# Optimization experiments

Hardware: AMD Instinct MI355X
Metric: run time of the kernel (lower is better)

## Reference

```python
import jax, jax.numpy as jnp
import numpy as np

B, L, T = 256, 512, 128


def setup_inputs() -> dict:
    key = jax.random.key(0)
    k1, k2, k3, k4, k5, k6 = jax.random.split(key, 6)
    inputs = jax.random.normal(k1, (B, L, T), dtype=jnp.float32)
    transitions = jax.random.normal(k2, (T, T), dtype=jnp.float32) * (2.0 / T) ** 0.5
    start_transitions = jax.random.normal(k3, (T,), dtype=jnp.float32)
    end_transitions = jax.random.normal(k4, (T,), dtype=jnp.float32)
    tags = jax.random.randint(k5, (B, L), 0, T, dtype=jnp.int32)
    lengths = jax.random.randint(k6, (B,), L // 2, L + 1, dtype=jnp.int32)
    mask = (jnp.arange(L)[None, :] < lengths[:, None]).astype(jnp.int32)
    return {"inputs": inputs, "transitions": transitions,
            "start_transitions": start_transitions, "end_transitions": end_transitions,
            "tags": tags, "mask": mask}


def _input_likelihood(logits, maskf, transitions, start_t, end_t):
    # logits [B,L,T], maskf [B,L] float
    alpha0 = start_t[None, :] + logits[:, 0]  # [B,T]

    def step(alpha, xs):
        emit, m = xs  # emit [B,T], m [B]
        inner = alpha[:, :, None] + emit[:, None, :] + transitions[None]  # [B,T,T]
        new_alpha = jax.nn.logsumexp(inner, axis=1)
        alpha = new_alpha * m[:, None] + alpha * (1.0 - m[:, None])
        return alpha, None

    xs = (jnp.swapaxes(logits[:, 1:], 0, 1), jnp.swapaxes(maskf[:, 1:], 0, 1))
    alpha, _ = jax.lax.scan(step, alpha0, xs)
    stops = alpha + end_t[None, :]
    return jax.nn.logsumexp(stops, axis=-1)  # [B]


def _joint_likelihood(logits, tags, maskf, transitions, start_t, end_t):
    b_idx = jnp.arange(logits.shape[0])
    score = start_t[tags[:, 0]]
    trans_scores = transitions[tags[:, :-1], tags[:, 1:]]  # [B,L-1]
    emit = jnp.take_along_axis(logits, tags[:, :, None], axis=2)[..., 0]  # [B,L]
    score = score + jnp.sum(trans_scores * maskf[:, 1:], axis=1)
    score = score + jnp.sum(emit[:, :-1] * maskf[:, :-1], axis=1)
    last_idx = jnp.sum(maskf, axis=1).astype(jnp.int32) - 1
    last_tags = tags[b_idx, last_idx]
    score = score + end_t[last_tags] + logits[:, -1][b_idx, last_tags] * maskf[:, -1]
    return score


def reference(inputs, transitions, start_transitions, end_transitions, tags, mask):
    maskf = mask.astype(inputs.dtype)
    log_den = _input_likelihood(inputs, maskf, transitions, start_transitions, end_transitions)
    log_num = _joint_likelihood(inputs, tags, maskf, transitions, start_transitions, end_transitions)
    return jnp.sum(log_num - log_den)
```

## Files before the change

kernel.cpp:

```cpp
#include <hip/hip_runtime.h>

#define BB 256
#define LL 512
#define TT 128
#define CH 16

typedef _Float16 h2 __attribute__((ext_vector_type(2)));

static __device__ inline h2 pkrtz(float a, float b) {
  return __builtin_bit_cast(h2, __builtin_amdgcn_cvt_pkrtz(a, b));
}

#if defined(__has_builtin)
#if __has_builtin(__builtin_amdgcn_fdot2)
#define FDOT2(a, b, c) __builtin_amdgcn_fdot2((a), (b), (c), false)
#endif
#endif
#ifndef FDOT2
static __device__ inline float fdot2_fb(h2 a, h2 b, float c) {
  return fmaf((float)a.x, (float)b.x, fmaf((float)a.y, (float)b.y, c));
}
#define FDOT2(a, b, c) fdot2_fb((a), (b), (c))
#endif

static __device__ inline float wave_max_dpp(float x) {
  int v = __float_as_int(x);
#define DPP_STEP(ctrl)                                                  \
  {                                                                     \
    int t = __builtin_amdgcn_update_dpp(v, v, (ctrl), 0xf, 0xf, false); \
    x = fmaxf(x, __int_as_float(t));                                    \
    v = __float_as_int(x);                                              \
  }
  DPP_STEP(0x111) DPP_STEP(0x112) DPP_STEP(0x114) DPP_STEP(0x118)
  DPP_STEP(0x142) DPP_STEP(0x143)
#undef DPP_STEP
  return __int_as_float(__builtin_amdgcn_readlane(v, 63));
}

static __device__ inline h2 bch2(unsigned u) { return __builtin_bit_cast(h2, u); }
static __device__ inline unsigned expbits(unsigned u) {
  return __float_as_uint(__expf(__uint_as_float(u)));
}

__global__ __launch_bounds__(256)
__attribute__((amdgpu_waves_per_eu(1, 1)))
void crf_fb_kernel(const float* __restrict__ inputs,
                   const float* __restrict__ trans,
                   const float* __restrict__ start_t,
                   const float* __restrict__ end_t,
                   const int* __restrict__ tags,
                   const int* __restrict__ mask,
                   float* __restrict__ diff) {
  const int b = blockIdx.x;
  const int tid = threadIdx.x;
  const int lane = tid & 63;
  const int wid = tid >> 6;

  __shared__ __align__(16) float fbuf[2][CH * TT];
  __shared__ __align__(16) float bbuf[2][CH * TT];
  __shared__ __align__(16) h2 g_lds[64];
  __shared__ float numA_sh, numB_sh;
  __shared__ int sb_sh;

  int lm = 0;
  const int* mk = mask + b * LL;
#pragma unroll
  for (int q = 0; q < LL / 64; ++q) lm += mk[q * 64 + lane];
#pragma unroll
  for (int d = 1; d < 64; d <<= 1) lm += __shfl_xor(lm, d);
  const int len = lm;
  const int m = (len - 1) >> 1;
  const int NC = (len - 1 - m + CH - 1) / CH;

  const float* erow = inputs + (size_t)b * LL * TT;
  const float2* er2 = (const float2*)erow;
  const float2* tr2 = (const float2*)trans;

  auto STAGE = [&](float* dst, const float* gbase) {
    const uint4* gs = (const uint4*)gbase;
    uint4* ds = (uint4*)dst;
    uint4 v[8];
#pragma unroll
    for (int q = 0; q < 8; ++q) v[q] = gs[q * 64 + lane];
#pragma unroll
    for (int q = 0; q < 8; ++q) {
      uint4 o;
      o.x = expbits(v[q].x);
      o.y = expbits(v[q].y);
      o.z = expbits(v[q].z);
      o.w = expbits(v[q].w);
      ds[q * 64 + lane] = o;
    }
  };

  int S = 0;
  float inv_sc = 1.0f;
  int cur_ex = 0;
  h2 Ea0[64], Ea1[64];
  h2 pk;

  if (wid == 0) {
#pragma unroll
    for (int p = 0; p < 64; ++p) {
      float2 r0 = tr2[(2 * p) * 64 + lane];
      float2 r1 = tr2[(2 * p + 1) * 64 + lane];
      h2 c0, c1;
      c0.x = (_Float16)__expf(r0.x);
      c0.y = (_Float16)__expf(r1.x);
      c1.x = (_Float16)__expf(r0.y);
      c1.y = (_Float16)__expf(r1.y);
      Ea0[p] = c0;
      Ea1[p] = c1;
    }
    float2 em0 = er2[lane];
    float f0 = __expf(start_t[2 * lane] + em0.x);
    float f1 = __expf(start_t[2 * lane + 1] + em0.y);
    pk = pkrtz(f0, f1);
    float mx = wave_max_dpp(fmaxf(f0, f1));
    int exm = (int)((__float_as_uint(mx) >> 23) & 255) - 127;
    inv_sc = __uint_as_float((unsigned)(120 - exm) << 23);
    cur_ex = exm + 7;
  } else if (wid == 1) {
#pragma unroll
    for (int p = 0; p < 64; ++p) {
      float2 r0 = tr2[(2 * lane) * 64 + p];
      float2 r1 = tr2[(2 * lane + 1) * 64 + p];
      h2 c0, c1;
      c0.x = (_Float16)__expf(r0.x);
      c0.y = (_Float16)__expf(r0.y);
      c1.x = (_Float16)__expf(r1.x);
      c1.y = (_Float16)__expf(r1.y);
      Ea0[p] = c0;
      Ea1[p] = c1;
    }
    float2 em = er2[(size_t)(len - 1) * 64 + lane];
    float g0 = __expf(end_t[2 * lane] + em.x);
    float g1 = __expf(end_t[2 * lane + 1] + em.y);
    pk = pkrtz(g0, g1);
    float mx = wave_max_dpp(fmaxf(g0, g1));
    int exm = (int)((__float_as_uint(mx) >> 23) & 255) - 127;
    inv_sc = __uint_as_float((unsigned)(120 - exm) << 23);
    cur_ex = exm + 7;
  } else if (wid == 2) {
    STAGE(fbuf[0], erow + 1 * TT);
    const int* tg = tags + (size_t)b * LL;
    const int hl = len >> 1;
    float sc = 0.f;
    for (int t = lane; t < hl; t += 64) {
      int cu = tg[t];
      sc += erow[(size_t)t * TT + cu];
      if (t >= 1) sc += trans[tg[t - 1] * TT + cu];
    }
    if (lane == 0) sc += start_t[tg[0]];
#pragma unroll
    for (int d = 1; d < 64; d <<= 1) sc += __shfl_xor(sc, d);
    if (lane == 0) numA_sh = sc;
  } else {
    STAGE(bbuf[0], erow + (size_t)(len - 1 - CH) * TT);
    const int* tg = tags + (size_t)b * LL;
    const int hl = len >> 1;
    float sc = 0.f;
    for (int t = hl + lane; t < len; t += 64) {
      int cu = tg[t];
      sc += erow[(size_t)t * TT + cu];
      sc += trans[tg[t - 1] * TT + cu];
    }
    if (lane == 0) sc += end_t[tg[len - 1]];
#pragma unroll
    for (int d = 1; d < 64; d <<= 1) sc += __shfl_xor(sc, d);
    if (lane == 0) numB_sh = sc;
  }

  __syncthreads();

  for (int c = 0; c < NC; ++c) {
    if (wid == 0) {
      const float2* emb = (const float2*)fbuf[c & 1];
      const int tbeg = 1 + CH * c;
      const int tend = min(tbeg + CH - 1, m);
#pragma unroll 1
      for (int t = tbeg; t <= tend; ++t) {
        float2 fe = emb[(t - tbeg) * 64 + lane];
        float f0 = fe.x * inv_sc;
        float f1 = fe.y * inv_sc;
        float a0 = 0.f, a1 = 0.f, a2 = 0.f, a3 = 0.f;
        float c0 = 0.f, c1 = 0.f, c2 = 0.f, c3 = 0.f;
        const int pki = (int)__builtin_bit_cast(unsigned, pk);
#pragma unroll
        for (int q = 0; q < 16; ++q) {
          h2 s0 = bch2((unsigned)__builtin_amdgcn_readlane(pki, 4 * q + 0));
          a0 = FDOT2(s0, Ea0[4 * q + 0], a0);
          c0 = FDOT2(s0, Ea1[4 * q + 0], c0);
          h2 s1 = bch2((unsigned)__builtin_amdgcn_readlane(pki, 4 * q + 1));
          a1 = FDOT2(s1, Ea0[4 * q + 1], a1);
          c1 = FDOT2(s1, Ea1[4 * q + 1], c1);
          h2 s2 = bch2((unsigned)__builtin_amdgcn_readlane(pki, 4 * q + 2));
          a2 = FDOT2(s2, Ea0[4 * q + 2], a2);
          c2 = FDOT2(s2, Ea1[4 * q + 2], c2);
          h2 s3 = bch2((unsigned)__builtin_amdgcn_readlane(pki, 4 * q + 3));
          a3 = FDOT2(s3, Ea0[4 * q + 3], a3);
          c3 = FDOT2(s3, Ea1[4 * q + 3], c3);
        }
        float w0 = ((a0 + a1) + (a2 + a3)) * f0;
        float w1 = ((c0 + c1) + (c2 + c3)) * f1;
        pk = pkrtz(w0, w1);
        S += cur_ex;
        float mx = wave_max_dpp(fmaxf(w0, w1));
        int exm = (int)((__float_as_uint(mx) >> 23) & 255) - 127;
        inv_sc = __uint_as_float((unsigned)(120 - exm) << 23);
        cur_ex = exm + 7;
      }
    } else if (wid == 1) {
      const int thi = len - 2 - CH * c;
      const int lb = len - 1 - CH * (c + 1);
      const int tlo = max(m, lb);
      const float2* emb = (const float2*)bbuf[c & 1];
#pragma unroll 1
      for (int t = thi; t >= tlo; --t) {
        float2 pe = emb[(t - lb) * 64 + lane];
        float a0 = 0.f, a1 = 0.f, a2 = 0.f, a3 = 0.f;
        float c0 = 0.f, c1 = 0.f, c2 = 0.f, c3 = 0.f;
        const int pki = (int)__builtin_bit_cast(unsigned, pk);
#pragma unroll
        for (int q = 0; q < 16; ++q) {
          h2 s0 = bch2((unsigned)__builtin_amdgcn_readlane(pki, 4 * q + 0));
          a0 = FDOT2(s0, Ea0[4 * q + 0], a0);
          c0 = FDOT2(s0, Ea1[4 * q + 0], c0);
          h2 s1 = bch2((unsigned)__builtin_amdgcn_readlane(pki, 4 * q + 1));
          a1 = FDOT2(s1, Ea0[4 * q + 1], a1);
          c1 = FDOT2(s1, Ea1[4 * q + 1], c1);
          h2 s2 = bch2((unsigned)__builtin_amdgcn_readlane(pki, 4 * q + 2));
          a2 = FDOT2(s2, Ea0[4 * q + 2], a2);
          c2 = FDOT2(s2, Ea1[4 * q + 2], c2);
          h2 s3 = bch2((unsigned)__builtin_amdgcn_readlane(pki, 4 * q + 3));
          a3 = FDOT2(s3, Ea0[4 * q + 3], a3);
          c3 = FDOT2(s3, Ea1[4 * q + 3], c3);
        }
        float v0 = (a0 + a1) + (a2 + a3);
        float v1 = (c0 + c1) + (c2 + c3);
        if (t > m) {
          v0 *= pe.x;
          v1 *= pe.y;
        }
        float w0 = v0 * inv_sc, w1 = v1 * inv_sc;
        pk = pkrtz(w0, w1);
        S += cur_ex;
        float mx = wave_max_dpp(fmaxf(w0, w1));
        int exm = (int)((__float_as_uint(mx) >> 23) & 255) - 127;
        inv_sc = __uint_as_float((unsigned)(120 - exm) << 23);
        cur_ex = exm + 7;
      }
    } else if (wid == 2) {
      if (c + 1 < NC) STAGE(fbuf[(c + 1) & 1], erow + (size_t)(1 + CH * (c + 1)) * TT);
    } else {
      if (c + 1 < NC) STAGE(bbuf[(c + 1) & 1], erow + (size_t)(len - 1 - CH * (c + 2)) * TT);
    }
    __syncthreads();
  }

  if (wid == 1) {
    g_lds[lane] = pk;
    if (lane == 0) sb_sh = S;
  }
  __syncthreads();

  if (wid == 0) {
    h2 a = pk;
    h2 g = g_lds[lane];
    float v = (float)a.x * (float)g.x + (float)a.y * (float)g.y;
#pragma unroll
    for (int d = 1; d < 64; d <<= 1) v += __shfl_xor(v, d);
    if (lane == 0) {
      float log_den = (float)(S + sb_sh) * 0.6931471805599453f + __logf(v);
      diff[b] = (numA_sh + numB_sh) - log_den;
    }
  }
}

__global__ void crf_sum_kernel(const float* __restrict__ diff,
                               float* __restrict__ out) {
  const int tid = threadIdx.x;
  float v = diff[tid];
#pragma unroll
  for (int d = 1; d < 64; d <<= 1) v += __shfl_xor(v, d);
  __shared__ float r[4];
  if ((tid & 63) == 0) r[tid >> 6] = v;
  __syncthreads();
  if (tid == 0) out[0] = r[0] + r[1] + r[2] + r[3];
}

extern "C" void kernel_launch(void* const* d_in, const int* in_sizes, int n_in,
                              void* d_out, int out_size, void* d_ws, size_t ws_size,
                              hipStream_t stream) {
  const float* inputs = (const float*)d_in[0];
  const float* trans = (const float*)d_in[1];
  const float* start_t = (const float*)d_in[2];
  const float* end_t = (const float*)d_in[3];
  const int* tags = (const int*)d_in[4];
  const int* mask = (const int*)d_in[5];
  float* diff = (float*)d_ws;
  float* out = (float*)d_out;

  crf_fb_kernel<<<BB, 256, 0, stream>>>(inputs, trans, start_t, end_t, tags,
                                        mask, diff);
  crf_sum_kernel<<<1, 256, 0, stream>>>(diff, out);
}
```

Baseline: 135.3 us.

## Replace readlane+fdot2 recurrence matvec with MFMA 16x16x32 f16 products

The per-step 128x128 matrix-vector product in the forward and backward recurrences moves from scalar readlane broadcasts feeding fdot2 chains onto MFMA 16x16x32 f16 instructions. The alpha/beta vector now round-trips through LDS each step and is broadcast as the A operand, with the exponentiated transition matrix held in registers in MFMA B-operand layout. This aims to cut the per-step VALU and readlane instruction count on the serial critical path. In exchange, only one row of each 16x16 MFMA output is useful, and every step adds LDS write/read latency plus MFMA pipeline latency.

Result: slower. 170.9 us (+26.3%).

```diff
diff --git a/kernel.cpp b/kernel.cpp
--- a/kernel.cpp
+++ b/kernel.cpp
@@ -6,22 +6,14 @@
 #define CH 16
 
 typedef _Float16 h2 __attribute__((ext_vector_type(2)));
+typedef _Float16 f16x8 __attribute__((ext_vector_type(8)));
+typedef float f32x4 __attribute__((ext_vector_type(4)));
+
+#define MFMA16x32(A, B, C) __builtin_amdgcn_mfma_f32_16x16x32_f16((A), (B), (C), 0, 0, 0)
 
 static __device__ inline h2 pkrtz(float a, float b) {
   return __builtin_bit_cast(h2, __builtin_amdgcn_cvt_pkrtz(a, b));
 }
-
-#if defined(__has_builtin)
-#if __has_builtin(__builtin_amdgcn_fdot2)
-#define FDOT2(a, b, c) __builtin_amdgcn_fdot2((a), (b), (c), false)
-#endif
-#endif
-#ifndef FDOT2
-static __device__ inline float fdot2_fb(h2 a, h2 b, float c) {
-  return fmaf((float)a.x, (float)b.x, fmaf((float)a.y, (float)b.y, c));
-}
-#define FDOT2(a, b, c) fdot2_fb((a), (b), (c))
-#endif
 
 static __device__ inline float wave_max_dpp(float x) {
   int v = __float_as_int(x);
@@ -37,7 +29,6 @@
   return __int_as_float(__builtin_amdgcn_readlane(v, 63));
 }
 
-static __device__ inline h2 bch2(unsigned u) { return __builtin_bit_cast(h2, u); }
 static __device__ inline unsigned expbits(unsigned u) {
   return __float_as_uint(__expf(__uint_as_float(u)));
 }
@@ -58,6 +49,7 @@
 
   __shared__ __align__(16) float fbuf[2][CH * TT];
   __shared__ __align__(16) float bbuf[2][CH * TT];
+  __shared__ __align__(16) h2 ef_lds[64];
   __shared__ __align__(16) h2 g_lds[64];
   __shared__ float numA_sh, numB_sh;
   __shared__ int sb_sh;
@@ -74,7 +66,6 @@
 
   const float* erow = inputs + (size_t)b * LL * TT;
   const float2* er2 = (const float2*)erow;
-  const float2* tr2 = (const float2*)trans;
 
   auto STAGE = [&](float* dst, const float* gbase) {
     const uint4* gs = (const uint4*)gbase;
@@ -96,47 +87,52 @@
   int S = 0;
   float inv_sc = 1.0f;
   int cur_ex = 0;
-  h2 Ea0[64], Ea1[64];
-  h2 pk;
+  f16x8 EB[8][4];
+  const int lg = lane >> 4, lc = lane & 15;
 
   if (wid == 0) {
 #pragma unroll
-    for (int p = 0; p < 64; ++p) {
-      float2 r0 = tr2[(2 * p) * 64 + lane];
-      float2 r1 = tr2[(2 * p + 1) * 64 + lane];
-      h2 c0, c1;
-      c0.x = (_Float16)__expf(r0.x);
-      c0.y = (_Float16)__expf(r1.x);
-      c1.x = (_Float16)__expf(r0.y);
-      c1.y = (_Float16)__expf(r1.y);
-      Ea0[p] = c0;
-      Ea1[p] = c1;
-    }
+    for (int n = 0; n < 8; ++n)
+#pragma unroll
+      for (int c = 0; c < 4; ++c) {
+        f16x8 e;
+#pragma unroll
+        for (int jj = 0; jj < 8; ++jj)
+          e[jj] = (_Float16)__expf(trans[(32 * c + 8 * lg + jj) * TT + 16 * n + lc]);
+        EB[n][c] = e;
+      }
     float2 em0 = er2[lane];
     float f0 = __expf(start_t[2 * lane] + em0.x);
     float f1 = __expf(start_t[2 * lane + 1] + em0.y);
-    pk = pkrtz(f0, f1);
+    ef_lds[lane] = pkrtz(f0, f1);
     float mx = wave_max_dpp(fmaxf(f0, f1));
     int exm = (int)((__float_as_uint(mx) >> 23) & 255) - 127;
     inv_sc = __uint_as_float((unsigned)(120 - exm) << 23);
     cur_ex = exm + 7;
   } else if (wid == 1) {
-#pragma unroll
-    for (int p = 0; p < 64; ++p) {
-      float2 r0 = tr2[(2 * lane) * 64 + p];
-      float2 r1 = tr2[(2 * lane + 1) * 64 + p];
-      h2 c0, c1;
-      c0.x = (_Float16)__expf(r0.x);
-      c0.y = (_Float16)__expf(r0.y);
-      c1.x = (_Float16)__expf(r1.x);
-      c1.y = (_Float16)__expf(r1.y);
-      Ea0[p] = c0;
-      Ea1[p] = c1;
-    }
+    const float2* tr2 = (const float2*)trans;
+#pragma unroll
+    for (int n = 0; n < 8; ++n)
+#pragma unroll
+      for (int c = 0; c < 4; ++c) {
+        int base = (16 * n + lc) * 64 + 16 * c + 4 * lg;
+        float2 r0 = tr2[base + 0], r1 = tr2[base + 1];
+        float2 r2 = tr2[base + 2], r3 = tr2[base + 3];
+        f16x8 e;
+        e[0] = (_Float16)__expf(r0.x);
+        e[1] = (_Float16)__expf(r0.y);
+        e[2] = (_Float16)__expf(r1.x);
+        e[3] = (_Float16)__expf(r1.y);
+        e[4] = (_Float16)__expf(r2.x);
+        e[5] = (_Float16)__expf(r2.y);
+        e[6] = (_Float16)__expf(r3.x);
+        e[7] = (_Float16)__expf(r3.y);
+        EB[n][c] = e;
+      }
     float2 em = er2[(size_t)(len - 1) * 64 + lane];
     float g0 = __expf(end_t[2 * lane] + em.x);
     float g1 = __expf(end_t[2 * lane + 1] + em.y);
-    pk = pkrtz(g0, g1);
+    g_lds[lane] = pkrtz(g0, g1);
     float mx = wave_max_dpp(fmaxf(g0, g1));
     int exm = (int)((__float_as_uint(mx) >> 23) & 255) - 127;
     inv_sc = __uint_as_float((unsigned)(120 - exm) << 23);
@@ -173,39 +169,46 @@
 
   __syncthreads();
 
+  const f32x4 z4 = {0.f, 0.f, 0.f, 0.f};
+
   for (int c = 0; c < NC; ++c) {
     if (wid == 0) {
-      const float2* emb = (const float2*)fbuf[c & 1];
+      const float* fb = fbuf[c & 1];
+      const uint4* ep = (const uint4*)ef_lds;
       const int tbeg = 1 + CH * c;
       const int tend = min(tbeg + CH - 1, m);
 #pragma unroll 1
       for (int t = tbeg; t <= tend; ++t) {
-        float2 fe = emb[(t - tbeg) * 64 + lane];
-        float f0 = fe.x * inv_sc;
-        float f1 = fe.y * inv_sc;
-        float a0 = 0.f, a1 = 0.f, a2 = 0.f, a3 = 0.f;
-        float c0 = 0.f, c1 = 0.f, c2 = 0.f, c3 = 0.f;
-        const int pki = (int)__builtin_bit_cast(unsigned, pk);
-#pragma unroll
-        for (int q = 0; q < 16; ++q) {
-          h2 s0 = bch2((unsigned)__builtin_amdgcn_readlane(pki, 4 * q + 0));
-          a0 = FDOT2(s0, Ea0[4 * q + 0], a0);
-          c0 = FDOT2(s0, Ea1[4 * q + 0], c0);
-          h2 s1 = bch2((unsigned)__builtin_amdgcn_readlane(pki, 4 * q + 1));
-          a1 = FDOT2(s1, Ea0[4 * q + 1], a1);
-          c1 = FDOT2(s1, Ea1[4 * q + 1], c1);
-          h2 s2 = bch2((unsigned)__builtin_amdgcn_readlane(pki, 4 * q + 2));
-          a2 = FDOT2(s2, Ea0[4 * q + 2], a2);
-          c2 = FDOT2(s2, Ea1[4 * q + 2], c2);
-          h2 s3 = bch2((unsigned)__builtin_amdgcn_readlane(pki, 4 * q + 3));
-          a3 = FDOT2(s3, Ea0[4 * q + 3], a3);
-          c3 = FDOT2(s3, Ea1[4 * q + 3], c3);
+        f16x8 A0 = __builtin_bit_cast(f16x8, ep[0 + lg]);
+        f16x8 A1 = __builtin_bit_cast(f16x8, ep[4 + lg]);
+        f16x8 A2 = __builtin_bit_cast(f16x8, ep[8 + lg]);
+        f16x8 A3 = __builtin_bit_cast(f16x8, ep[12 + lg]);
+        float fv[8];
+        const int fbase = (t - tbeg) * TT + lc;
+#pragma unroll
+        for (int n = 0; n < 8; ++n) fv[n] = fb[fbase + 16 * n];
+        f32x4 acc[8];
+#pragma unroll
+        for (int n = 0; n < 8; ++n) acc[n] = MFMA16x32(A0, EB[n][0], z4);
+#pragma unroll
+        for (int n = 0; n < 8; ++n) acc[n] = MFMA16x32(A1, EB[n][1], acc[n]);
+#pragma unroll
+        for (int n = 0; n < 8; ++n) acc[n] = MFMA16x32(A2, EB[n][2], acc[n]);
+#pragma unroll
+        for (int n = 0; n < 8; ++n) acc[n] = MFMA16x32(A3, EB[n][3], acc[n]);
+        float w[8];
+#pragma unroll
+        for (int n = 0; n < 8; ++n) w[n] = acc[n][0] * (fv[n] * inv_sc);
+        float wm = w[0];
+#pragma unroll
+        for (int n = 1; n < 8; ++n) wm = fmaxf(wm, w[n]);
+        if (lane < 16) {
+          _Float16* sp = (_Float16*)ef_lds;
+#pragma unroll
+          for (int n = 0; n < 8; ++n) sp[16 * n + lc] = pkrtz(w[n], w[n]).x;
         }
-        float w0 = ((a0 + a1) + (a2 + a3)) * f0;
-        float w1 = ((c0 + c1) + (c2 + c3)) * f1;
-        pk = pkrtz(w0, w1);
         S += cur_ex;
-        float mx = wave_max_dpp(fmaxf(w0, w1));
+        float mx = wave_max_dpp(wm);
         int exm = (int)((__float_as_uint(mx) >> 23) & 255) - 127;
         inv_sc = __uint_as_float((unsigned)(120 - exm) << 23);
         cur_ex = exm + 7;
@@ -214,38 +217,45 @@
       const int thi = len - 2 - CH * c;
       const int lb = len - 1 - CH * (c + 1);
       const int tlo = max(m, lb);
-      const float2* emb = (const float2*)bbuf[c & 1];
+      const float* bbm = bbuf[c & 1];
+      const uint4* gp = (const uint4*)g_lds;
 #pragma unroll 1
       for (int t = thi; t >= tlo; --t) {
-        float2 pe = emb[(t - lb) * 64 + lane];
-        float a0 = 0.f, a1 = 0.f, a2 = 0.f, a3 = 0.f;
-        float c0 = 0.f, c1 = 0.f, c2 = 0.f, c3 = 0.f;
-        const int pki = (int)__builtin_bit_cast(unsigned, pk);
-#pragma unroll
-        for (int q = 0; q < 16; ++q) {
-          h2 s0 = bch2((unsigned)__builtin_amdgcn_readlane(pki, 4 * q + 0));
-          a0 = FDOT2(s0, Ea0[4 * q + 0], a0);
-          c0 = FDOT2(s0, Ea1[4 * q + 0], c0);
-          h2 s1 = bch2((unsigned)__builtin_amdgcn_readlane(pki, 4 * q + 1));
-          a1 = FDOT2(s1, Ea0[4 * q + 1], a1);
-          c1 = FDOT2(s1, Ea1[4 * q + 1], c1);
-          h2 s2 = bch2((unsigned)__builtin_amdgcn_readlane(pki, 4 * q + 2));
-          a2 = FDOT2(s2, Ea0[4 * q + 2], a2);
-          c2 = FDOT2(s2, Ea1[4 * q + 2], c2);
-          h2 s3 = bch2((unsigned)__builtin_amdgcn_readlane(pki, 4 * q + 3));
-          a3 = FDOT2(s3, Ea0[4 * q + 3], a3);
-          c3 = FDOT2(s3, Ea1[4 * q + 3], c3);
+        f16x8 A0 = __builtin_bit_cast(f16x8, gp[0 + lg]);
+        f16x8 A1 = __builtin_bit_cast(f16x8, gp[4 + lg]);
+        f16x8 A2 = __builtin_bit_cast(f16x8, gp[8 + lg]);
+        f16x8 A3 = __builtin_bit_cast(f16x8, gp[12 + lg]);
+        float pex[8];
+        const int pbase = (t - lb) * TT + lc;
+#pragma unroll
+        for (int n = 0; n < 8; ++n) pex[n] = bbm[pbase + 16 * n];
+        f32x4 acc[8];
+#pragma unroll
+        for (int n = 0; n < 8; ++n) acc[n] = MFMA16x32(A0, EB[n][0], z4);
+#pragma unroll
+        for (int n = 0; n < 8; ++n) acc[n] = MFMA16x32(A1, EB[n][1], acc[n]);
+#pragma unroll
+        for (int n = 0; n < 8; ++n) acc[n] = MFMA16x32(A2, EB[n][2], acc[n]);
+#pragma unroll
+        for (int n = 0; n < 8; ++n) acc[n] = MFMA16x32(A3, EB[n][3], acc[n]);
+        float w[8];
+        if (t > m) {
+#pragma unroll
+          for (int n = 0; n < 8; ++n) w[n] = acc[n][0] * (pex[n] * inv_sc);
+        } else {
+#pragma unroll
+          for (int n = 0; n < 8; ++n) w[n] = acc[n][0] * inv_sc;
         }
-        float v0 = (a0 + a1) + (a2 + a3);
-        float v1 = (c0 + c1) + (c2 + c3);
-        if (t > m) {
-          v0 *= pe.x;
-          v1 *= pe.y;
+        float wm = w[0];
+#pragma unroll
+        for (int n = 1; n < 8; ++n) wm = fmaxf(wm, w[n]);
+        if (lane < 16) {
+          _Float16* sp = (_Float16*)g_lds;
+#pragma unroll
+          for (int n = 0; n < 8; ++n) sp[16 * n + lc] = pkrtz(w[n], w[n]).x;
         }
-        float w0 = v0 * inv_sc, w1 = v1 * inv_sc;
-        pk = pkrtz(w0, w1);
         S += cur_ex;
-        float mx = wave_max_dpp(fmaxf(w0, w1));
+        float mx = wave_max_dpp(wm);
         int exm = (int)((__float_as_uint(mx) >> 23) & 255) - 127;
         inv_sc = __uint_as_float((unsigned)(120 - exm) << 23);
         cur_ex = exm + 7;
@@ -258,14 +268,11 @@
     __syncthreads();
   }
 
-  if (wid == 1) {
-    g_lds[lane] = pk;
-    if (lane == 0) sb_sh = S;
-  }
+  if (wid == 1 && lane == 0) sb_sh = S;
   __syncthreads();
 
   if (wid == 0) {
-    h2 a = pk;
+    h2 a = ef_lds[lane];
     h2 g = g_lds[lane];
     float v = (float)a.x * (float)g.x + (float)a.y * (float)g.y;
 #pragma unroll
```
